# Kernel optimization log

Hardware: AMD Instinct MI355X
Metric: run time of the kernel (lower is better)

The kernel has to match this reference:

```python
import jax, jax.numpy as jnp
import numpy as np

B, N, D, DE, E, L = 8, 4096, 128, 128, 262144, 2
FF = 4 * D  # feedforward hidden


def _ln(x, g, b, eps=1e-5):
    m = jnp.mean(x, axis=-1, keepdims=True)
    v = jnp.mean(jnp.square(x - m), axis=-1, keepdims=True)
    return (x - m) * jax.lax.rsqrt(v + eps) * g + b


def setup_inputs() -> dict:
    key = jax.random.key(0)
    ks = iter(jax.random.split(key, 40))

    def w(shape):
        fan_in = shape[-2]
        return jax.random.normal(next(ks), shape, jnp.float32) / np.sqrt(fan_in)

    return {
        "x": jax.random.normal(next(ks), (B, N, D), jnp.float32),
        "edge_index": jax.random.randint(next(ks), (2, E), 0, B * N, dtype=jnp.int32),
        "edge_attr": jax.random.normal(next(ks), (E, DE), jnp.float32),
        # message MLP (n_message = 3 linears)
        "msg_W0": w((L, 2 * D + DE, D)), "msg_b0": jnp.zeros((L, D)),
        "msg_W1": w((L, D, D)), "msg_b1": jnp.zeros((L, D)),
        "msg_W2": w((L, D, D)), "msg_b2": jnp.zeros((L, D)),
        "norm0_g": jnp.ones((L, D)), "norm0_b": jnp.zeros((L, D)),
        # feedforward
        "ff_W0": w((L, D, FF)), "ff_b0": jnp.zeros((L, FF)),
        "ff_W1": w((L, FF, D)), "ff_b1": jnp.zeros((L, D)),
        "norm1_g": jnp.ones((L, D)), "norm1_b": jnp.zeros((L, D)),
        # edge update MLP (n_edge_gvps = 3 linears)
        "edge_W0": w((L, 2 * D + DE, DE)), "edge_b0": jnp.zeros((L, DE)),
        "edge_W1": w((L, DE, DE)), "edge_b1": jnp.zeros((L, DE)),
        "edge_W2": w((L, DE, DE)), "edge_b2": jnp.zeros((L, DE)),
        "enorm_g": jnp.ones((L, DE)), "enorm_b": jnp.zeros((L, DE)),
    }


def reference(x, edge_index, edge_attr,
              msg_W0, msg_b0, msg_W1, msg_b1, msg_W2, msg_b2,
              norm0_g, norm0_b, ff_W0, ff_b0, ff_W1, ff_b1, norm1_g, norm1_b,
              edge_W0, edge_b0, edge_W1, edge_b1, edge_W2, edge_b2,
              enorm_g, enorm_b):
    Bx, Nx, Dx = x.shape
    n_nodes = Bx * Nx
    nodes = x.reshape(n_nodes, Dx)          # torch.flatten(x, 0, 1)
    src, dst = edge_index[0], edge_index[1]
    # in-degree for mean aggregation (guard isolated nodes)
    deg = jax.ops.segment_sum(jnp.ones((edge_attr.shape[0],), nodes.dtype), dst,
                              num_segments=n_nodes)
    inv_deg = (1.0 / jnp.maximum(deg, 1.0))[:, None]

    n_layers = msg_W0.shape[0]
    for l in range(n_layers):
        # --- node message passing (mean aggr at dst) ---
        h = jnp.concatenate([nodes[src], edge_attr, nodes[dst]], axis=-1)  # [E, 2D+DE]
        m = jax.nn.relu(h @ msg_W0[l] + msg_b0[l])
        m = jax.nn.relu(m @ msg_W1[l] + msg_b1[l])
        m = m @ msg_W2[l] + msg_b2[l]
        agg = jax.ops.segment_sum(m, dst, num_segments=n_nodes) * inv_deg
        nodes = _ln(nodes + agg, norm0_g[l], norm0_b[l])
        # --- feedforward ---
        ff = jax.nn.relu(nodes @ ff_W0[l] + ff_b0[l]) @ ff_W1[l] + ff_b1[l]
        nodes = _ln(nodes + ff, norm1_g[l], norm1_b[l])
        # --- edge update ---
        eh = jnp.concatenate([nodes[src], edge_attr, nodes[dst]], axis=-1)
        e = jax.nn.relu(eh @ edge_W0[l] + edge_b0[l])
        e = jax.nn.relu(e @ edge_W1[l] + edge_b1[l])
        e = e @ edge_W2[l] + edge_b2[l]
        edge_attr = _ln(edge_attr + e, enorm_g[l], enorm_b[l])

    return nodes.reshape(Bx, Nx, Dx)
```

## Files before the change

kernel.cpp:

```cpp
#include <hip/hip_runtime.h>

#define E_      262144
#define NNODES  32768
#define L_      2

typedef __attribute__((ext_vector_type(8))) short  bf16x8;
typedef __attribute__((ext_vector_type(4))) float  f32x4;

typedef __attribute__((address_space(1))) const unsigned int gu32;
typedef __attribute__((address_space(3))) unsigned int       lu32;

__device__ __forceinline__ void gl16(const void* g, void* l) {
    __builtin_amdgcn_global_load_lds((gu32*)g, (lu32*)l, 16, 0, 0);
}

__device__ __forceinline__ float bf2f(unsigned short u) {
    union { unsigned int i; float f; } v; v.i = ((unsigned int)u) << 16; return v.f;
}
__device__ __forceinline__ unsigned short f2bf(float f) {
    union { float f; unsigned int i; } v; v.f = f;
    unsigned int r = v.i + 0x7FFFu + ((v.i >> 16) & 1u);
    return (unsigned short)(r >> 16);
}

__global__ __launch_bounds__(256)
void k_cvt2(const float* __restrict__ a, unsigned short* __restrict__ oa, int n4a,
            const float* __restrict__ b, unsigned short* __restrict__ ob, int n4b)
{
    int i = blockIdx.x * 256 + threadIdx.x;
    if (i < n4a) {
        float4 v = reinterpret_cast<const float4*>(a)[i];
        ushort4 o; o.x = f2bf(v.x); o.y = f2bf(v.y); o.z = f2bf(v.z); o.w = f2bf(v.w);
        reinterpret_cast<ushort4*>(oa)[i] = o;
    } else if (i < n4a + n4b) {
        int j = i - n4a;
        float4 v = reinterpret_cast<const float4*>(b)[j];
        ushort4 o; o.x = f2bf(v.x); o.y = f2bf(v.y); o.z = f2bf(v.z); o.w = f2bf(v.w);
        reinterpret_cast<ushort4*>(ob)[j] = o;
    }
}

struct TD  { const float* s; unsigned short* d; int off; int K; int nsh; };
struct TDA { TD v[13]; int total; };

__global__ __launch_bounds__(256)
void k_transpose_all(TDA t)
{
    int idx = blockIdx.x * 256 + threadIdx.x;
    if (idx >= t.total) return;
    int j = 0;
#pragma unroll
    for (int m = 1; m < 13; ++m) if (idx >= t.v[m].off) j = m;
    const TD& td = t.v[j];
    int local = idx - td.off;
    int k = local >> td.nsh;
    int n = local & ((1 << td.nsh) - 1);
    td.d[(size_t)n * td.K + k] = f2bf(td.s[local]);
}

template<bool LNEPI>
__global__ __launch_bounds__(256, 4)
void fused_mlp3(const unsigned short* __restrict__ nodes,
                const unsigned short* __restrict__ eattr,
                const int*            __restrict__ ei,
                const unsigned short* __restrict__ W0T,
                const unsigned short* __restrict__ W1T,
                const unsigned short* __restrict__ W2T,
                const float* __restrict__ b0, const float* __restrict__ b1,
                const float* __restrict__ b2,
                const float* __restrict__ g,  const float* __restrict__ bb,
                unsigned short* __restrict__ out)
{
    __shared__ unsigned short S0[64 * 64];
    __shared__ unsigned short SB[128 * 64];
    __shared__ unsigned short H [64 * 128];

    const int tid  = threadIdx.x;
    const int lane = tid & 63;
    const int w    = tid >> 6;
    const int wr   = w >> 1, wc = w & 1;
    const int m0   = blockIdx.x * 64;

    const int lrow = lane >> 3;
    const int soff = ((lane & 7) ^ lrow) * 8;

    char* S0c = (char*)S0;
    char* SBc = (char*)SB;
    char* Hc  = (char*)H;

    const unsigned short *pS[2], *pD[2], *pE[2];
#pragma unroll
    for (int i = 0; i < 2; ++i) {
        int r = w * 16 + i * 8 + lrow;
        int e = m0 + r;
        pS[i] = nodes + (size_t)ei[e]      * 128 + soff;
        pD[i] = nodes + (size_t)ei[E_ + e] * 128 + soff;
        pE[i] = eattr + (size_t)e          * 128 + soff;
    }

    f32x4 acc[2][4];
    auto zacc = [&]() {
#pragma unroll
        for (int m = 0; m < 2; ++m)
#pragma unroll
            for (int n = 0; n < 4; ++n) acc[m][n] = (f32x4){0.f, 0.f, 0.f, 0.f};
    };

    auto mma = [&](const char* Ab, int abytes, int kbase) {
#pragma unroll
        for (int ks = 0; ks < 2; ++ks) {
            const int kb = (kbase + ks * 32) * 2 + (lane >> 4) * 16;
            bf16x8 a[2], b[4];
#pragma unroll
            for (int m = 0; m < 2; ++m) {
                int row = wr * 32 + m * 16 + (lane & 15);
                a[m] = *reinterpret_cast<const bf16x8*>(Ab + row * abytes + (kb ^ ((row & 7) << 4)));
            }
            const int kbb = ks * 64 + (lane >> 4) * 16;
#pragma unroll
            for (int n = 0; n < 4; ++n) {
                int row = wc * 64 + n * 16 + (lane & 15);
                b[n] = *reinterpret_cast<const bf16x8*>(SBc + row * 128 + (kbb ^ ((row & 7) << 4)));
            }
#pragma unroll
            for (int m = 0; m < 2; ++m)
#pragma unroll
                for (int n = 0; n < 4; ++n)
                    acc[m][n] = __builtin_amdgcn_mfma_f32_16x16x32_bf16(a[m], b[n], acc[m][n], 0, 0, 0);
        }
    };

    auto towrite = [&](const float* bias) {
#pragma unroll
        for (int n = 0; n < 4; ++n) {
            int cg = wc * 64 + n * 16 + (lane & 15);
            float bi = bias[cg];
#pragma unroll
            for (int m = 0; m < 2; ++m) {
#pragma unroll
                for (int j = 0; j < 4; ++j) {
                    int rg = wr * 32 + m * 16 + (lane >> 4) * 4 + j;
                    float v = fmaxf(acc[m][n][j] + bi, 0.f);
                    *(unsigned short*)(Hc + rg * 256 + ((2 * cg) ^ ((rg & 7) << 4))) = f2bf(v);
                }
            }
        }
    };

    zacc();
    for (int k0 = 0; k0 < 384; k0 += 64) {
#pragma unroll
        for (int i = 0; i < 2; ++i) {
            const unsigned short* pa = (k0 < 128 ? pS[i] : (k0 < 256 ? pE[i] : pD[i])) + (k0 & 64);
            gl16(pa, S0c + (w * 16 + i * 8) * 128);
        }
#pragma unroll
        for (int i = 0; i < 4; ++i)
            gl16(W0T + (size_t)(w * 32 + i * 8 + lrow) * 384 + k0 + soff,
                 SBc + (w * 32 + i * 8) * 128);
        __syncthreads();
        mma(S0c, 128, 0);
        __syncthreads();
    }
    towrite(b0);
    zacc();
#pragma unroll
    for (int k0 = 0; k0 < 128; k0 += 64) {
#pragma unroll
        for (int i = 0; i < 4; ++i)
            gl16(W1T + (size_t)(w * 32 + i * 8 + lrow) * 128 + k0 + soff,
                 SBc + (w * 32 + i * 8) * 128);
        __syncthreads();
        mma(Hc, 256, k0);
        __syncthreads();
    }
    towrite(b1);
    zacc();
#pragma unroll
    for (int k0 = 0; k0 < 128; k0 += 64) {
#pragma unroll
        for (int i = 0; i < 4; ++i)
            gl16(W2T + (size_t)(w * 32 + i * 8 + lrow) * 128 + k0 + soff,
                 SBc + (w * 32 + i * 8) * 128);
        __syncthreads();
        mma(Hc, 256, k0);
        __syncthreads();
    }

    if (!LNEPI) {
#pragma unroll
        for (int n = 0; n < 4; ++n) {
            int cg = wc * 64 + n * 16 + (lane & 15);
            float bi = b2[cg];
#pragma unroll
            for (int m = 0; m < 2; ++m) {
                int rg = m0 + wr * 32 + m * 16 + (lane >> 4) * 4;
                unsigned short* cp = out + (size_t)rg * 128 + cg;
#pragma unroll
                for (int j = 0; j < 4; ++j)
                    cp[(size_t)j * 128] = f2bf(acc[m][n][j] + bi);
            }
        }
    } else {
#pragma unroll
        for (int n = 0; n < 4; ++n) {
            int cg = wc * 64 + n * 16 + (lane & 15);
            float bi = b2[cg];
#pragma unroll
            for (int m = 0; m < 2; ++m) {
#pragma unroll
                for (int j = 0; j < 4; ++j) {
                    int rg = m0 + wr * 32 + m * 16 + (lane >> 4) * 4 + j;
                    acc[m][n][j] += bi + bf2f(eattr[(size_t)rg * 128 + cg]);
                }
            }
        }
        float* ps = (float*)SBc;
        float* pq = ps + 128;
#pragma unroll
        for (int m = 0; m < 2; ++m) {
#pragma unroll
            for (int j = 0; j < 4; ++j) {
                float s = 0.f, q = 0.f;
#pragma unroll
                for (int n = 0; n < 4; ++n) {
                    float v = acc[m][n][j];
                    s += v; q += v * v;
                }
#pragma unroll
                for (int msk = 1; msk < 16; msk <<= 1) {
                    s += __shfl_xor(s, msk);
                    q += __shfl_xor(q, msk);
                }
                if ((lane & 15) == 0) {
                    int rl = wr * 32 + m * 16 + (lane >> 4) * 4 + j;
                    ps[wc * 64 + rl] = s;
                    pq[wc * 64 + rl] = q;
                }
            }
        }
        __syncthreads();
#pragma unroll
        for (int m = 0; m < 2; ++m) {
#pragma unroll
            for (int j = 0; j < 4; ++j) {
                int rl = wr * 32 + m * 16 + (lane >> 4) * 4 + j;
                float S = ps[rl] + ps[64 + rl];
                float Q = pq[rl] + pq[64 + rl];
                float mean = S * (1.f / 128.f);
                float var  = Q * (1.f / 128.f) - mean * mean;
                float rs   = rsqrtf(var + 1e-5f);
                int rg = m0 + rl;
#pragma unroll
                for (int n = 0; n < 4; ++n) {
                    int cg = wc * 64 + n * 16 + (lane & 15);
                    out[(size_t)rg * 128 + cg] =
                        f2bf((acc[m][n][j] - mean) * rs * g[cg] + bb[cg]);
                }
            }
        }
    }
}

template<int BM, int K, int NTOT, bool RELU>
__global__ __launch_bounds__(256)
void mlp_gemm(const unsigned short* __restrict__ Abase,
              const unsigned short* __restrict__ WT,
              const float*          __restrict__ bias,
              unsigned short*       __restrict__ C)
{
    constexpr int MI = BM / 32;
    __shared__ unsigned short Alds[BM * 64];
    __shared__ unsigned short Blds[128 * 64];

    const int tid  = threadIdx.x;
    const int lane = tid & 63;
    const int w    = tid >> 6;
    const int wr   = w >> 1, wc = w & 1;
    const int m0   = blockIdx.x * BM;
    const int n0   = blockIdx.y * 128;

    const int lrow = lane >> 3;
    const int soff = ((lane & 7) ^ lrow) * 8;

    const unsigned short *pS[MI], *pB[4];
#pragma unroll
    for (int i = 0; i < MI; ++i)
        pS[i] = Abase + (size_t)(m0 + w * (BM / 4) + i * 8 + lrow) * K + soff;
#pragma unroll
    for (int i = 0; i < 4; ++i)
        pB[i] = WT + (size_t)(n0 + w * 32 + i * 8 + lrow) * K + soff;

    f32x4 acc[MI][4];
#pragma unroll
    for (int m = 0; m < MI; ++m)
#pragma unroll
        for (int n = 0; n < 4; ++n) acc[m][n] = (f32x4){0.f, 0.f, 0.f, 0.f};

#pragma unroll
    for (int k0 = 0; k0 < K; k0 += 64) {
#pragma unroll
        for (int i = 0; i < MI; ++i)
            gl16(pS[i] + k0, Alds + (w * (BM / 4) + i * 8) * 64);
#pragma unroll
        for (int i = 0; i < 4; ++i)
            gl16(pB[i] + k0, Blds + (w * 32 + i * 8) * 64);
        __syncthreads();

#pragma unroll
        for (int ks = 0; ks < 2; ++ks) {
            const int kb = ks * 64 + (lane >> 4) * 16;
            bf16x8 a[MI], b[4];
#pragma unroll
            for (int m = 0; m < MI; ++m) {
                int row = wr * (BM / 2) + m * 16 + (lane & 15);
                a[m] = *reinterpret_cast<const bf16x8*>(
                    (const char*)Alds + row * 128 + (kb ^ ((row & 7) << 4)));
            }
#pragma unroll
            for (int n = 0; n < 4; ++n) {
                int row = wc * 64 + n * 16 + (lane & 15);
                b[n] = *reinterpret_cast<const bf16x8*>(
                    (const char*)Blds + row * 128 + (kb ^ ((row & 7) << 4)));
            }
#pragma unroll
            for (int m = 0; m < MI; ++m)
#pragma unroll
                for (int n = 0; n < 4; ++n)
                    acc[m][n] = __builtin_amdgcn_mfma_f32_16x16x32_bf16(a[m], b[n], acc[m][n], 0, 0, 0);
        }
        __syncthreads();
    }

#pragma unroll
    for (int n = 0; n < 4; ++n) {
        int colg = n0 + wc * 64 + n * 16 + (lane & 15);
        float bi = bias[colg];
#pragma unroll
        for (int m = 0; m < MI; ++m) {
            int rowg = m0 + wr * (BM / 2) + m * 16 + (lane >> 4) * 4;
            unsigned short* cp = C + (size_t)rowg * NTOT + colg;
#pragma unroll
            for (int j = 0; j < 4; ++j) {
                float r = acc[m][n][j] + bi;
                if (RELU) r = fmaxf(r, 0.f);
                cp[(size_t)j * NTOT] = f2bf(r);
            }
        }
    }
}

template<bool F32OUT>
__global__ __launch_bounds__(256)
void ff1_ln(const unsigned short* __restrict__ Abase,
            const unsigned short* __restrict__ WT,
            const float* __restrict__ bias,
            const unsigned short* __restrict__ resid,
            const float* __restrict__ g, const float* __restrict__ bb,
            void* __restrict__ outp)
{
    constexpr int K = 512;
    __shared__ unsigned short Alds[64 * 64];
    __shared__ unsigned short Blds[128 * 64];

    const int tid  = threadIdx.x;
    const int lane = tid & 63;
    const int w    = tid >> 6;
    const int wr   = w >> 1, wc = w & 1;
    const int m0   = blockIdx.x * 64;

    const int lrow = lane >> 3;
    const int soff = ((lane & 7) ^ lrow) * 8;

    const unsigned short *pS[2], *pB[4];
#pragma unroll
    for (int i = 0; i < 2; ++i)
        pS[i] = Abase + (size_t)(m0 + w * 16 + i * 8 + lrow) * K + soff;
#pragma unroll
    for (int i = 0; i < 4; ++i)
        pB[i] = WT + (size_t)(w * 32 + i * 8 + lrow) * K + soff;

    f32x4 acc[2][4];
#pragma unroll
    for (int m = 0; m < 2; ++m)
#pragma unroll
        for (int n = 0; n < 4; ++n) acc[m][n] = (f32x4){0.f, 0.f, 0.f, 0.f};

#pragma unroll
    for (int k0 = 0; k0 < K; k0 += 64) {
#pragma unroll
        for (int i = 0; i < 2; ++i)
            gl16(pS[i] + k0, Alds + (w * 16 + i * 8) * 64);
#pragma unroll
        for (int i = 0; i < 4; ++i)
            gl16(pB[i] + k0, Blds + (w * 32 + i * 8) * 64);
        __syncthreads();

#pragma unroll
        for (int ks = 0; ks < 2; ++ks) {
            const int kb = ks * 64 + (lane >> 4) * 16;
            bf16x8 a[2], b[4];
#pragma unroll
            for (int m = 0; m < 2; ++m) {
                int row = wr * 32 + m * 16 + (lane & 15);
                a[m] = *reinterpret_cast<const bf16x8*>(
                    (const char*)Alds + row * 128 + (kb ^ ((row & 7) << 4)));
            }
#pragma unroll
            for (int n = 0; n < 4; ++n) {
                int row = wc * 64 + n * 16 + (lane & 15);
                b[n] = *reinterpret_cast<const bf16x8*>(
                    (const char*)Blds + row * 128 + (kb ^ ((row & 7) << 4)));
            }
#pragma unroll
            for (int m = 0; m < 2; ++m)
#pragma unroll
                for (int n = 0; n < 4; ++n)
                    acc[m][n] = __builtin_amdgcn_mfma_f32_16x16x32_bf16(a[m], b[n], acc[m][n], 0, 0, 0);
        }
        __syncthreads();
    }

#pragma unroll
    for (int n = 0; n < 4; ++n) {
        int cg = wc * 64 + n * 16 + (lane & 15);
        float bi = bias[cg];
#pragma unroll
        for (int m = 0; m < 2; ++m) {
#pragma unroll
            for (int j = 0; j < 4; ++j) {
                int rg = m0 + wr * 32 + m * 16 + (lane >> 4) * 4 + j;
                acc[m][n][j] += bi + bf2f(resid[(size_t)rg * 128 + cg]);
            }
        }
    }
    float* ps = (float*)Blds;
    float* pq = ps + 128;
#pragma unroll
    for (int m = 0; m < 2; ++m) {
#pragma unroll
        for (int j = 0; j < 4; ++j) {
            float s = 0.f, q = 0.f;
#pragma unroll
            for (int n = 0; n < 4; ++n) {
                float v = acc[m][n][j];
                s += v; q += v * v;
            }
#pragma unroll
            for (int msk = 1; msk < 16; msk <<= 1) {
                s += __shfl_xor(s, msk);
                q += __shfl_xor(q, msk);
            }
            if ((lane & 15) == 0) {
                int rl = wr * 32 + m * 16 + (lane >> 4) * 4 + j;
                ps[wc * 64 + rl] = s;
                pq[wc * 64 + rl] = q;
            }
        }
    }
    __syncthreads();
#pragma unroll
    for (int m = 0; m < 2; ++m) {
#pragma unroll
        for (int j = 0; j < 4; ++j) {
            int rl = wr * 32 + m * 16 + (lane >> 4) * 4 + j;
            float S = ps[rl] + ps[64 + rl];
            float Q = pq[rl] + pq[64 + rl];
            float mean = S * (1.f / 128.f);
            float var  = Q * (1.f / 128.f) - mean * mean;
            float rs   = rsqrtf(var + 1e-5f);
            int rg = m0 + rl;
#pragma unroll
            for (int n = 0; n < 4; ++n) {
                int cg = wc * 64 + n * 16 + (lane & 15);
                float y = (acc[m][n][j] - mean) * rs * g[cg] + bb[cg];
                if (F32OUT) ((float*)outp)[(size_t)rg * 128 + cg] = y;
                else ((unsigned short*)outp)[(size_t)rg * 128 + cg] = f2bf(y);
            }
        }
    }
}

__global__ __launch_bounds__(256)
void k_deg(const int* __restrict__ ei, int* __restrict__ deg)
{
    int e = blockIdx.x * 256 + threadIdx.x;
    atomicAdd(&deg[ei[E_ + e]], 1);
}

__global__ __launch_bounds__(1024)
void k_scan(const int* __restrict__ deg, int* __restrict__ off)
{
    __shared__ int part[1024];
    const int t = threadIdx.x;
    const int base = t * 32;
    int loc[32];
    int s = 0;
#pragma unroll
    for (int i = 0; i < 32; ++i) { loc[i] = s; s += deg[base + i]; }
    part[t] = s;
    __syncthreads();
    for (int d = 1; d < 1024; d <<= 1) {
        int v = (t >= d) ? part[t - d] : 0;
        __syncthreads();
        part[t] += v;
        __syncthreads();
    }
    const int pre = (t == 0) ? 0 : part[t - 1];
#pragma unroll
    for (int i = 0; i < 32; ++i) off[base + i] = pre + loc[i];
    if (t == 1023) off[NNODES] = pre + s;
}

__global__ __launch_bounds__(256)
void k_bucket(const int* __restrict__ ei, int* __restrict__ cursor, int* __restrict__ elist)
{
    int e = blockIdx.x * 256 + threadIdx.x;
    int d = ei[E_ + e];
    int pos = atomicAdd(&cursor[d], 1);
    elist[pos] = e;
}

__global__ __launch_bounds__(256)
void k_aggln(const unsigned short* __restrict__ m,
             const int* __restrict__ off, const int* __restrict__ elist,
             const unsigned short* __restrict__ nodes_in,
             const float* __restrict__ g, const float* __restrict__ bb,
             unsigned short* __restrict__ nodes_out)
{
    const int v    = blockIdx.x * 4 + (threadIdx.x >> 6);
    const int lane = threadIdx.x & 63;
    const int c    = lane * 2;
    const int beg  = off[v], end = off[v + 1];

    float a0 = 0.f, a1 = 0.f;
    for (int i = beg; i < end; ++i) {
        int e = elist[i];
        unsigned int u = *reinterpret_cast<const unsigned int*>(m + (size_t)e * 128 + c);
        a0 += bf2f((unsigned short)(u & 0xffffu));
        a1 += bf2f((unsigned short)(u >> 16));
    }
    const float inv = 1.f / fmaxf((float)(end - beg), 1.f);
    const size_t o = (size_t)v * 128 + c;
    float x0 = bf2f(nodes_in[o])     + a0 * inv;
    float x1 = bf2f(nodes_in[o + 1]) + a1 * inv;

    float s = x0 + x1, sq = x0 * x0 + x1 * x1;
#pragma unroll
    for (int mm = 1; mm < 64; mm <<= 1) { s += __shfl_xor(s, mm); sq += __shfl_xor(sq, mm); }
    float mean = s * (1.f / 128.f);
    float var  = sq * (1.f / 128.f) - mean * mean;
    float rs   = rsqrtf(var + 1e-5f);
    nodes_out[o]     = f2bf((x0 - mean) * rs * g[c]     + bb[c]);
    nodes_out[o + 1] = f2bf((x1 - mean) * rs * g[c + 1] + bb[c + 1]);
}

extern "C" void kernel_launch(void* const* d_in, const int* in_sizes, int n_in,
                              void* d_out, int out_size, void* d_ws, size_t ws_size,
                              hipStream_t stream)
{
    const float* x      = (const float*)d_in[0];
    const int*   ei     = (const int*)d_in[1];
    const float* eat0   = (const float*)d_in[2];
    const float* msg_W0 = (const float*)d_in[3];
    const float* msg_b0 = (const float*)d_in[4];
    const float* msg_W1 = (const float*)d_in[5];
    const float* msg_b1 = (const float*)d_in[6];
    const float* msg_W2 = (const float*)d_in[7];
    const float* msg_b2 = (const float*)d_in[8];
    const float* n0g    = (const float*)d_in[9];
    const float* n0b    = (const float*)d_in[10];
    const float* ff_W0  = (const float*)d_in[11];
    const float* ff_b0  = (const float*)d_in[12];
    const float* ff_W1  = (const float*)d_in[13];
    const float* ff_b1  = (const float*)d_in[14];
    const float* n1g    = (const float*)d_in[15];
    const float* n1b    = (const float*)d_in[16];
    const float* e_W0   = (const float*)d_in[17];
    const float* e_b0   = (const float*)d_in[18];
    const float* e_W1   = (const float*)d_in[19];
    const float* e_b1   = (const float*)d_in[20];
    const float* e_W2   = (const float*)d_in[21];
    const float* e_b2   = (const float*)d_in[22];
    const float* eng    = (const float*)d_in[23];
    const float* enb    = (const float*)d_in[24];

    char* ws = (char*)d_ws;
    const size_t MB = (size_t)1 << 20;
    unsigned short* nodes = (unsigned short*)(ws);
    unsigned short* edgec = (unsigned short*)(ws + 8 * MB);
    unsigned short* tmpA  = (unsigned short*)(ws + 72 * MB);
    unsigned short* ffh   = (unsigned short*)(ws + 136 * MB);
    unsigned short* wt    = (unsigned short*)(ws + 200 * MB);
    int*            deg   = (int*)(ws + 202 * MB);
    int*            off   = (int*)(ws + 202 * MB + 256 * 1024);
    int*            cur   = (int*)(ws + 202 * MB + 512 * 1024);
    int*            elist = (int*)(ws + 202 * MB + 768 * 1024);

    unsigned short* p = wt;
    unsigned short *wt_m0[L_], *wt_m1[L_], *wt_m2[L_], *wt_f0[L_], *wt_f1[L_];
    for (int l = 0; l < L_; ++l) {
        wt_m0[l] = p; p += 384 * 128;
        wt_m1[l] = p; p += 128 * 128;
        wt_m2[l] = p; p += 128 * 128;
        wt_f0[l] = p; p += 128 * 512;
        wt_f1[l] = p; p += 512 * 128;
    }
    unsigned short* wt_e0 = p; p += 384 * 128;
    unsigned short* wt_e1 = p; p += 128 * 128;
    unsigned short* wt_e2 = p; p += 128 * 128;

    TDA tda; int toff = 0, ti = 0;
    auto addT = [&](const float* s, unsigned short* d, int K, int N) {
        tda.v[ti++] = TD{s, d, toff, K, (N == 512 ? 9 : 7)};
        toff += K * N;
    };
    for (int l = 0; l < L_; ++l) {
        addT(msg_W0 + l * 384 * 128, wt_m0[l], 384, 128);
        addT(msg_W1 + l * 128 * 128, wt_m1[l], 128, 128);
        addT(msg_W2 + l * 128 * 128, wt_m2[l], 128, 128);
        addT(ff_W0  + l * 128 * 512, wt_f0[l], 128, 512);
        addT(ff_W1  + l * 512 * 128, wt_f1[l], 512, 128);
    }
    addT(e_W0, wt_e0, 384, 128);
    addT(e_W1, wt_e1, 128, 128);
    addT(e_W2, wt_e2, 128, 128);
    tda.total = toff;
    k_transpose_all<<<(toff + 255) / 256, 256, 0, stream>>>(tda);

    const int n4a = NNODES * 128 / 4, n4b = E_ * 128 / 4;
    k_cvt2<<<(n4a + n4b + 255) / 256, 256, 0, stream>>>(x, nodes, n4a, eat0, edgec, n4b);

    hipMemsetAsync(deg, 0, NNODES * sizeof(int), stream);
    k_deg<<<E_ / 256, 256, 0, stream>>>(ei, deg);
    k_scan<<<1, 1024, 0, stream>>>(deg, off);
    hipMemcpyAsync(cur, off, NNODES * sizeof(int), hipMemcpyDeviceToDevice, stream);
    k_bucket<<<E_ / 256, 256, 0, stream>>>(ei, cur, elist);

    const dim3 gE(E_ / 64, 1), gN64(NNODES / 64, 1), gF0(NNODES / 128, 4);

    for (int l = 0; l < L_; ++l) {
        fused_mlp3<false><<<gE, 256, 0, stream>>>(nodes, edgec, ei,
            wt_m0[l], wt_m1[l], wt_m2[l],
            msg_b0 + l * 128, msg_b1 + l * 128, msg_b2 + l * 128,
            nullptr, nullptr, tmpA);
        k_aggln<<<NNODES / 4, 256, 0, stream>>>(tmpA, off, elist, nodes,
            n0g + l * 128, n0b + l * 128, nodes);
        mlp_gemm<128, 128, 512, true><<<gF0, 256, 0, stream>>>(nodes, wt_f0[l], ff_b0 + l * 512, ffh);
        if (l == L_ - 1) {
            ff1_ln<true ><<<gN64, 256, 0, stream>>>(ffh, wt_f1[l], ff_b1 + l * 128,
                nodes, n1g + l * 128, n1b + l * 128, d_out);
        } else {
            ff1_ln<false><<<gN64, 256, 0, stream>>>(ffh, wt_f1[l], ff_b1 + l * 128,
                nodes, n1g + l * 128, n1b + l * 128, nodes);
        }
        if (l == 0) {
            fused_mlp3<true><<<gE, 256, 0, stream>>>(nodes, edgec, ei,
                wt_e0, wt_e1, wt_e2, e_b0, e_b1, e_b2, eng, enb, edgec);
        }
    }
}
```

Measured before the change: 453.2 us.

## Load gathered node/edge A-operands directly into registers, drop LDS staging buffer

The first GEMM of the fused MLP now gathers src/edge/dst rows straight from global memory into MFMA A-fragment registers instead of staging them through a shared-memory tile. This removes the S0 LDS buffer, which cuts LDS use and allows the occupancy hint to rise from 4 to 5 blocks per CU. The cost is that each wave does duplicated, less coalesced 16-byte global gathers. Those loads are not shared across the two column-waves, so global traffic and register pressure may go up.

Result: slower. 585.6 us (+29.2%).

```diff
diff --git a/kernel.cpp b/kernel.cpp
--- a/kernel.cpp
+++ b/kernel.cpp
@@ -59,7 +59,7 @@
 }
 
 template<bool LNEPI>
-__global__ __launch_bounds__(256, 4)
+__global__ __launch_bounds__(256, 5)
 void fused_mlp3(const unsigned short* __restrict__ nodes,
                 const unsigned short* __restrict__ eattr,
                 const int*            __restrict__ ei,
@@ -71,7 +71,6 @@
                 const float* __restrict__ g,  const float* __restrict__ bb,
                 unsigned short* __restrict__ out)
 {
-    __shared__ unsigned short S0[64 * 64];
     __shared__ unsigned short SB[128 * 64];
     __shared__ unsigned short H [64 * 128];
 
@@ -84,18 +83,17 @@
     const int lrow = lane >> 3;
     const int soff = ((lane & 7) ^ lrow) * 8;
 
-    char* S0c = (char*)S0;
     char* SBc = (char*)SB;
     char* Hc  = (char*)H;
 
-    const unsigned short *pS[2], *pD[2], *pE[2];
-#pragma unroll
-    for (int i = 0; i < 2; ++i) {
-        int r = w * 16 + i * 8 + lrow;
-        int e = m0 + r;
-        pS[i] = nodes + (size_t)ei[e]      * 128 + soff;
-        pD[i] = nodes + (size_t)ei[E_ + e] * 128 + soff;
-        pE[i] = eattr + (size_t)e          * 128 + soff;
+    const int koff = (lane >> 4) * 8;
+    const unsigned short *aS[2], *aD[2], *aE[2];
+#pragma unroll
+    for (int m = 0; m < 2; ++m) {
+        int e = m0 + wr * 32 + m * 16 + (lane & 15);
+        aS[m] = nodes + (size_t)ei[e]      * 128 + koff;
+        aD[m] = nodes + (size_t)ei[E_ + e] * 128 + koff;
+        aE[m] = eattr + (size_t)e          * 128 + koff;
     }
 
     f32x4 acc[2][4];
@@ -106,7 +104,14 @@
             for (int n = 0; n < 4; ++n) acc[m][n] = (f32x4){0.f, 0.f, 0.f, 0.f};
     };
 
-    auto mma = [&](const char* Ab, int abytes, int kbase) {
+    auto stageW = [&](const unsigned short* WT, int Kr, int k0) {
+#pragma unroll
+        for (int i = 0; i < 4; ++i)
+            gl16(WT + (size_t)(w * 32 + i * 8 + lrow) * Kr + k0 + soff,
+                 SBc + (w * 32 + i * 8) * 128);
+    };
+
+    auto mmaH = [&](int kbase) {
 #pragma unroll
         for (int ks = 0; ks < 2; ++ks) {
             const int kb = (kbase + ks * 32) * 2 + (lane >> 4) * 16;
@@ -114,7 +119,7 @@
 #pragma unroll
             for (int m = 0; m < 2; ++m) {
                 int row = wr * 32 + m * 16 + (lane & 15);
-                a[m] = *reinterpret_cast<const bf16x8*>(Ab + row * abytes + (kb ^ ((row & 7) << 4)));
+                a[m] = *reinterpret_cast<const bf16x8*>(Hc + row * 256 + (kb ^ ((row & 7) << 4)));
             }
             const int kbb = ks * 64 + (lane >> 4) * 16;
 #pragma unroll
@@ -148,42 +153,53 @@
     };
 
     zacc();
-    for (int k0 = 0; k0 < 384; k0 += 64) {
-#pragma unroll
-        for (int i = 0; i < 2; ++i) {
-            const unsigned short* pa = (k0 < 128 ? pS[i] : (k0 < 256 ? pE[i] : pD[i])) + (k0 & 64);
-            gl16(pa, S0c + (w * 16 + i * 8) * 128);
-        }
-#pragma unroll
-        for (int i = 0; i < 4; ++i)
-            gl16(W0T + (size_t)(w * 32 + i * 8 + lrow) * 384 + k0 + soff,
-                 SBc + (w * 32 + i * 8) * 128);
-        __syncthreads();
-        mma(S0c, 128, 0);
+#pragma unroll
+    for (int t = 0; t < 6; ++t) {
+        stageW(W0T, 384, t * 64);
+        bf16x8 areg[2][2];
+        const unsigned short* base[2];
+#pragma unroll
+        for (int m = 0; m < 2; ++m)
+            base[m] = (t < 2 ? aS[m] : (t < 4 ? aE[m] : aD[m])) + (t & 1) * 64;
+#pragma unroll
+        for (int ks = 0; ks < 2; ++ks)
+#pragma unroll
+            for (int m = 0; m < 2; ++m)
+                areg[ks][m] = *reinterpret_cast<const bf16x8*>(base[m] + ks * 32);
+        __syncthreads();
+#pragma unroll
+        for (int ks = 0; ks < 2; ++ks) {
+            const int kbb = ks * 64 + (lane >> 4) * 16;
+            bf16x8 b[4];
+#pragma unroll
+            for (int n = 0; n < 4; ++n) {
+                int row = wc * 64 + n * 16 + (lane & 15);
+                b[n] = *reinterpret_cast<const bf16x8*>(SBc + row * 128 + (kbb ^ ((row & 7) << 4)));
+            }
+#pragma unroll
+            for (int m = 0; m < 2; ++m)
+#pragma unroll
+                for (int n = 0; n < 4; ++n)
+                    acc[m][n] = __builtin_amdgcn_mfma_f32_16x16x32_bf16(areg[ks][m], b[n], acc[m][n], 0, 0, 0);
+        }
         __syncthreads();
     }
     towrite(b0);
     zacc();
 #pragma unroll
     for (int k0 = 0; k0 < 128; k0 += 64) {
-#pragma unroll
-        for (int i = 0; i < 4; ++i)
-            gl16(W1T + (size_t)(w * 32 + i * 8 + lrow) * 128 + k0 + soff,
-                 SBc + (w * 32 + i * 8) * 128);
-        __syncthreads();
-        mma(Hc, 256, k0);
+        stageW(W1T, 128, k0);
+        __syncthreads();
+        mmaH(k0);
         __syncthreads();
     }
     towrite(b1);
     zacc();
 #pragma unroll
     for (int k0 = 0; k0 < 128; k0 += 64) {
-#pragma unroll
-        for (int i = 0; i < 4; ++i)
-            gl16(W2T + (size_t)(w * 32 + i * 8 + lrow) * 128 + k0 + soff,
-                 SBc + (w * 32 + i * 8) * 128);
-        __syncthreads();
-        mma(Hc, 256, k0);
+        stageW(W2T, 128, k0);
+        __syncthreads();
+        mmaH(k0);
         __syncthreads();
     }
 
```
